# Optimization experiments

Measured on AMD Instinct MI355X. Metric: run time of the kernel, lower is better.

Reference implementation:

```python
import jax, jax.numpy as jnp
import numpy as np


def _knn_graph(x, k):
    """Faithful port of DynamicLstmGnn.knn_to_graph + get_u_v, returning the
    dense symmetrized edge-weight matrix [N, N] (the original re-sparsifies
    this same matrix via coalesce; nonzero extraction is data-dependent and
    not jit-able, so the dense matrix is the canonical output)."""
    N = x.shape[0]
    # negative squared euclidean distance: -||xi||^2 + 2 xi.xj - ||xj||^2
    xx = jnp.sum(x * x, axis=1, keepdims=True)          # [N, 1]
    inner = -2.0 * (x @ x.T)                              # [N, N]
    pairwise_distance = -xx - inner - xx.T                # [N, N], <= 0
    vals, idx = jax.lax.top_k(pairwise_distance, k)       # [N, k] largest (= closest)
    rows = jnp.repeat(jnp.arange(N), k)                   # idx_prime.flatten()
    # sparse COO -> to_dense (duplicate indices sum, matching torch.sparse)
    edges = jnp.zeros((N, N), dtype=x.dtype).at[rows, idx.ravel()].add(vals.ravel())
    edges_int = (edges > 0).astype(x.dtype)
    reflected_int = edges_int + edges_int.T
    reflected_edges = edges + edges.T
    denom = jnp.where(reflected_int == 0, jnp.ones((), x.dtype), reflected_int)
    edges = reflected_edges / denom
    diag = jnp.arange(N)
    edges = edges.at[diag, diag].set(0.0)                 # fill_diagonal_(0)
    return edges


def setup_inputs() -> dict:
    key = jax.random.key(0)
    x = jax.random.normal(key, (10000, 64), dtype=jnp.float32)
    return {"x": x, "k": 5}


def reference(x, k):
    return _knn_graph(x, k)
```

## Files before the change

### kernel.cpp

```cpp
#include <hip/hip_runtime.h>
#include <math.h>
#include <limits.h>

#define D 64
#define K 5
#define LK 8
#define GK 12
#define NSPLIT 16
#define NTILES 625
#define ROWBLK 157
#define NCOMP (ROWBLK * NSPLIT)
typedef unsigned int u32;
typedef unsigned long long u64;
typedef __bf16 bf16x8 __attribute__((ext_vector_type(8)));
typedef float  f32x4v __attribute__((ext_vector_type(4)));

__device__ __forceinline__ u32 med3u(u32 a, u32 b, u32 c) {
    u32 r;
    asm("v_med3_u32 %0, %1, %2, %3" : "=v"(r) : "v"(a), "v"(b), "v"(c));
    return r;
}

__device__ __forceinline__ u32 pack32(float v, int idx) {
    u32 u = __float_as_uint(v);
    u ^= ((u32)((int)u >> 31)) | 0x80000000u;
    return (u & 0xFFFFC000u) | ((~(u32)idx) & 0x3FFFu);
}
__device__ __forceinline__ int idx32(u32 key) { return (int)((~key) & 0x3FFFu); }

__device__ __forceinline__ u64 packKV(float v, int idx) {
    u32 u = __float_as_uint(v);
    u ^= ((u32)((int)u >> 31)) | 0x80000000u;
    return ((u64)u << 32) | (u32)(~idx);
}
__device__ __forceinline__ float unpackV(u64 key) {
    u32 hu = (u32)(key >> 32);
    return (hu & 0x80000000u) ? __uint_as_float(hu & 0x7fffffffu)
                              : __uint_as_float(~hu);
}

template<int LO, int LA, int LB, typename T>
__device__ __forceinline__ void mergeKeep(T a[LA], const T b[LB]) {
    T A[LA], B[LB], out[LO];
#pragma unroll
    for (int i = 0; i < LA; ++i) A[i] = a[i];
#pragma unroll
    for (int i = 0; i < LB; ++i) B[i] = b[i];
#pragma unroll
    for (int m = 0; m < LO; ++m) {
        bool ta = A[0] >= B[0];
        out[m] = ta ? A[0] : B[0];
#pragma unroll
        for (int i = 0; i < LA - 1; ++i) A[i] = ta ? A[i + 1] : A[i];
        A[LA - 1] = ta ? (T)0 : A[LA - 1];
#pragma unroll
        for (int i = 0; i < LB - 1; ++i) B[i] = ta ? B[i] : B[i + 1];
        B[LB - 1] = ta ? B[LB - 1] : (T)0;
    }
#pragma unroll
    for (int m = 0; m < LO; ++m) a[m] = out[m];
}

__global__ __launch_bounds__(256) void prep(
    const float* __restrict__ x, __bf16* __restrict__ xbA, float* __restrict__ xxf, int N)
{
    int g = blockIdx.x * 256 + threadIdx.x;
    const int REPACK = NTILES * 2 * 64;
    if (g < REPACK) {
        int tile = g >> 7;
        int rem  = g & 127;
        int kh   = rem >> 6;
        int lane = rem & 63;
        int q = lane >> 4, r = lane & 15;
        int row = tile * 16 + r;
        int k0  = kh * 32 + q * 8;
        const float4* p = (const float4*)(x + (size_t)row * D + k0);
        float4 v0 = p[0], v1 = p[1];
        bf16x8 o;
        o[0] = (__bf16)v0.x; o[1] = (__bf16)v0.y; o[2] = (__bf16)v0.z; o[3] = (__bf16)v0.w;
        o[4] = (__bf16)v1.x; o[5] = (__bf16)v1.y; o[6] = (__bf16)v1.z; o[7] = (__bf16)v1.w;
        ((bf16x8*)xbA)[g] = o;
        return;
    }
    int i = g - REPACK;
    if (i >= N) return;
    const float4* p = (const float4*)(x + (size_t)i * D);
    float s = 0.f;
#pragma unroll
    for (int t = 0; t < 16; ++t) {
        float4 v = p[t];
        s += v.x * v.x + v.y * v.y + v.z * v.z + v.w * v.w;
    }
    xxf[i] = s;
}

__global__ __launch_bounds__(256) void topk_zero_mfma(
    const __bf16* __restrict__ xbA, const float* __restrict__ xxf, int N,
    u32* __restrict__ wsK, float* __restrict__ outZ, long long totalF4,
    int nZero, int f4PerZ)
{
    const int bx  = blockIdx.x;
    const int tid = threadIdx.x;

    if (bx % 6 == 0) {
        int zid = bx / 6;
        if (zid >= nZero) return;
        long long s = (long long)zid * f4PerZ;
        long long e = s + f4PerZ; if (e > totalF4) e = totalF4;
        const f32x4v z = {0.f, 0.f, 0.f, 0.f};
        for (long long i = s + tid; i < e; i += 256)
            __builtin_nontemporal_store(z, (f32x4v*)(outZ + 4 * i));
        return;
    }

    const int cid = bx - (bx / 6 + 1);
    if (cid >= NCOMP) return;
    const int split = cid / ROWBLK;
    const int rb    = cid - split * ROWBLK;

    const int lane = tid & 63;
    const int wave = tid >> 6;
    const int l15  = lane & 15;
    const int q    = lane >> 4;
    const int r0 = rb * 64 + wave * 16;

    const bf16x8* fb = (const bf16x8*)xbA;

    int bt = r0 >> 4; if (bt > NTILES - 1) bt = NTILES - 1;
    const bf16x8 B0 = fb[bt * 128 + lane];
    const bf16x8 B1 = fb[bt * 128 + 64 + lane];

    const bf16x8* ap = fb + (size_t)split * 128 + lane;
    const float* xcp = xxf + split * 16 + q * 4;
    int cbase = split * 16 + q * 4;
    const int apBump = NSPLIT * 128;
    const int xcBump = NSPLIT * 16;

    u32 L[LK];
#pragma unroll
    for (int m = 0; m < LK; ++m) L[m] = 0u;

    for (int t = split; t < NTILES; t += NSPLIT) {
        const bf16x8 A0 = ap[0];
        const bf16x8 A1 = ap[64];
        const f32x4v xc = *(const f32x4v*)xcp;
        ap += apBump;
        xcp += xcBump;

        f32x4v acc = {0.f, 0.f, 0.f, 0.f};
        acc = __builtin_amdgcn_mfma_f32_16x16x32_bf16(A0, B0, acc, 0, 0, 0);
        acc = __builtin_amdgcn_mfma_f32_16x16x32_bf16(A1, B1, acc, 0, 0, 0);

#pragma unroll
        for (int v = 0; v < 4; ++v) {
            float dk = fmaf(-0.5f, xc[v], acc[v]);
            u32 key = pack32(dk, cbase + v);
            u32 n0 = max(L[0], key);
            u32 n1 = med3u(L[0], L[1], key);
            u32 n2 = med3u(L[1], L[2], key);
            u32 n3 = med3u(L[2], L[3], key);
            u32 n4 = med3u(L[3], L[4], key);
            u32 n5 = med3u(L[4], L[5], key);
            u32 n6 = med3u(L[5], L[6], key);
            u32 n7 = med3u(L[6], L[7], key);
            L[0]=n0; L[1]=n1; L[2]=n2; L[3]=n3; L[4]=n4; L[5]=n5; L[6]=n6; L[7]=n7;
        }
        cbase += xcBump;
    }

#pragma unroll
    for (int mask = 16; mask <= 32; mask <<= 1) {
        u32 P[LK];
#pragma unroll
        for (int m = 0; m < LK; ++m) P[m] = (u32)__shfl_xor((int)L[m], mask);
        mergeKeep<LK, LK, LK, u32>(L, P);
    }

    if (lane < 16) {
        int row = r0 + l15;
        if (row < N) {
            u32* dst = wsK + ((size_t)row * NSPLIT + split) * LK;
#pragma unroll
            for (int m = 0; m < LK; ++m) dst[m] = L[m];
        }
    }
}

__global__ __launch_bounds__(256) void rescore_scatter(
    const u32* __restrict__ wsK, const float* __restrict__ x, const float* __restrict__ xxf,
    float* __restrict__ out, int N)
{
    const int lane = threadIdx.x & 63;
    const int wave = threadIdx.x >> 6;
    const int sub  = lane & 3;
    const int row  = blockIdx.x * 64 + wave * 16 + (lane >> 2);
    const bool vrow = (row < N);
    const int rr = vrow ? row : 0;

    u32 cur[GK];
    {
        const u32* Lp = wsK + ((size_t)rr * NSPLIT + 4 * sub) * LK;
#pragma unroll
        for (int m = 0; m < LK; ++m) cur[m] = Lp[m];
#pragma unroll
        for (int m = LK; m < GK; ++m) cur[m] = 0u;
#pragma unroll
        for (int l = 1; l < 4; ++l) {
            u32 b[LK];
#pragma unroll
            for (int m = 0; m < LK; ++m) b[m] = Lp[l * LK + m];
            mergeKeep<GK, GK, LK, u32>(cur, b);
        }
    }
#pragma unroll
    for (int mask = 1; mask <= 2; mask <<= 1) {
        u32 P[GK];
#pragma unroll
        for (int m = 0; m < GK; ++m) P[m] = (u32)__shfl_xor((int)cur[m], mask);
        mergeKeep<GK, GK, GK, u32>(cur, P);
    }

    const float nxi = xxf[rr];
    int   cj[3]; bool cval[3];
    float d[3] = {0.f, 0.f, 0.f};
    const f32x4v* pj[3];
#pragma unroll
    for (int c = 0; c < 3; ++c) {
        int j = idx32(cur[sub * 3 + c]);
        cval[c] = (j < N) && (cur[sub * 3 + c] != 0u);
        cj[c] = cval[c] ? j : 0;
        pj[c] = (const f32x4v*)(x + (size_t)cj[c] * D);
    }
    const f32x4v* xip = (const f32x4v*)(x + (size_t)rr * D);
#pragma unroll
    for (int t = 0; t < 16; ++t) {
        const f32x4v xv = xip[t];
#pragma unroll
        for (int c = 0; c < 3; ++c) {
            const f32x4v pv = pj[c][t];
            d[c] = fmaf(xv[0], pv[0], d[c]);
            d[c] = fmaf(xv[1], pv[1], d[c]);
            d[c] = fmaf(xv[2], pv[2], d[c]);
            d[c] = fmaf(xv[3], pv[3], d[c]);
        }
    }
    u64 F[K];
#pragma unroll
    for (int c = 0; c < 3; ++c) {
        float val = 2.f * d[c] - nxi - xxf[cj[c]];
        F[c] = cval[c] ? packKV(val, cj[c]) : 0ull;
    }
    F[3] = 0ull; F[4] = 0ull;
    { u64 a0=F[0],a1=F[1],a2=F[2];
      if (a0 < a1) { u64 t0=a0; a0=a1; a1=t0; }
      if (a1 < a2) { u64 t0=a1; a1=a2; a2=t0; }
      if (a0 < a1) { u64 t0=a0; a0=a1; a1=t0; }
      F[0]=a0; F[1]=a1; F[2]=a2; }
#pragma unroll
    for (int mask = 1; mask <= 2; mask <<= 1) {
        u64 P[K];
#pragma unroll
        for (int m = 0; m < K; ++m) P[m] = __shfl_xor(F[m], mask);
        mergeKeep<K, K, K, u64>(F, P);
    }

    if (sub == 0 && vrow) {
#pragma unroll
        for (int m = 0; m < K; ++m) {
            int j = (int)(~(u32)F[m]);
            if ((unsigned)j < (unsigned)N && j != row) {
                float v = unpackV(F[m]);
                atomicAdd(out + (size_t)row * N + j, v);
                atomicAdd(out + (size_t)j * N + row, v);
            }
        }
    }
}

extern "C" void kernel_launch(void* const* d_in, const int* in_sizes, int n_in,
                              void* d_out, int out_size, void* d_ws, size_t ws_size,
                              hipStream_t stream) {
    const float* x = (const float*)d_in[0];
    const int N = in_sizes[0] / D;
    float* out = (float*)d_out;

    const size_t oXB = 0;
    const size_t oXX = ((size_t)NTILES * 2 * 64 * 8 * 2 + 255) & ~255ull;
    const size_t oWK = (oXX + (size_t)N * 4 + 255) & ~255ull;
    __bf16* xbA = (__bf16*)((char*)d_ws + oXB);
    float*  xxf = (float*)((char*)d_ws + oXX);
    u32*    wsK = (u32*)((char*)d_ws + oWK);

    const int prepThreads = NTILES * 2 * 64 + N;
    prep<<<(prepThreads + 255) / 256, 256, 0, stream>>>(x, xbA, xxf, N);

    long long totalF4 = (long long)out_size / 4;
    const int nBlocksTotal = 3024;
    const int nZero = (nBlocksTotal + 5) / 6;
    int f4PerZ = (int)((totalF4 + nZero - 1) / nZero);
    topk_zero_mfma<<<nBlocksTotal, 256, 0, stream>>>(
        xbA, xxf, N, wsK, out, totalF4, nZero, f4PerZ);

    rescore_scatter<<<ROWBLK, 256, 0, stream>>>(wsK, x, xxf, out, N);
}
```

Measured before the change: 451.2 us.

## Fuse top-k and rescore-scatter kernels with atomic-counter grid dependency

Merges the top-k/zeroing kernel and the rescore/scatter kernel into one launch. The trailing 157 blocks spin on two global completion counters, reset in prep, until all zeroing and top-k blocks have signalled. This removes one kernel launch boundary and the tail gap between them. In exchange it relies on forward progress of block scheduling: if the spinning blocks occupy slots ahead of producers they can delay them or deadlock. The threadfence plus atomic handshake also adds some overhead.

After: 951.7 us. 2.11x slower.

```diff
diff --git a/kernel.cpp b/kernel.cpp
--- a/kernel.cpp
+++ b/kernel.cpp
@@ -10,6 +10,8 @@
 #define NTILES 625
 #define ROWBLK 157
 #define NCOMP (ROWBLK * NSPLIT)
+#define NMIX  3024
+#define NZERO 504
 typedef unsigned int u32;
 typedef unsigned long long u64;
 typedef __bf16 bf16x8 __attribute__((ext_vector_type(8)));
@@ -62,9 +64,11 @@
 }
 
 __global__ __launch_bounds__(256) void prep(
-    const float* __restrict__ x, __bf16* __restrict__ xbA, float* __restrict__ xxf, int N)
+    const float* __restrict__ x, __bf16* __restrict__ xbA, float* __restrict__ xxf,
+    u32* __restrict__ ctrs, int N)
 {
     int g = blockIdx.x * 256 + threadIdx.x;
+    if (g < 2) ctrs[g] = 0u;
     const int REPACK = NTILES * 2 * 64;
     if (g < REPACK) {
         int tile = g >> 7;
@@ -94,108 +98,122 @@
     xxf[i] = s;
 }
 
-__global__ __launch_bounds__(256) void topk_zero_mfma(
-    const __bf16* __restrict__ xbA, const float* __restrict__ xxf, int N,
-    u32* __restrict__ wsK, float* __restrict__ outZ, long long totalF4,
-    int nZero, int f4PerZ)
+__global__ __launch_bounds__(256) void fused(
+    const __bf16* __restrict__ xbA, const float* __restrict__ xxf,
+    const float* __restrict__ x, int N,
+    u32* __restrict__ wsK, u32* __restrict__ ctrs,
+    float* __restrict__ outZ, long long totalF4, int f4PerZ)
 {
     const int bx  = blockIdx.x;
     const int tid = threadIdx.x;
 
-    if (bx % 6 == 0) {
+    if (bx < NMIX && bx % 6 == 0) {
         int zid = bx / 6;
-        if (zid >= nZero) return;
         long long s = (long long)zid * f4PerZ;
         long long e = s + f4PerZ; if (e > totalF4) e = totalF4;
         const f32x4v z = {0.f, 0.f, 0.f, 0.f};
         for (long long i = s + tid; i < e; i += 256)
             __builtin_nontemporal_store(z, (f32x4v*)(outZ + 4 * i));
+        __threadfence();
+        __syncthreads();
+        if (tid == 0) atomicAdd(&ctrs[0], 1u);
         return;
     }
 
-    const int cid = bx - (bx / 6 + 1);
-    if (cid >= NCOMP) return;
-    const int split = cid / ROWBLK;
-    const int rb    = cid - split * ROWBLK;
-
+    if (bx < NMIX) {
+        const int cid = bx - (bx / 6 + 1);
+        if (cid >= NCOMP) { __syncthreads(); if (tid == 0) atomicAdd(&ctrs[1], 1u); return; }
+        const int split = cid / ROWBLK;
+        const int rb    = cid - split * ROWBLK;
+
+        const int lane = tid & 63;
+        const int wave = tid >> 6;
+        const int l15  = lane & 15;
+        const int q    = lane >> 4;
+        const int r0 = rb * 64 + wave * 16;
+
+        const bf16x8* fb = (const bf16x8*)xbA;
+
+        int bt = r0 >> 4; if (bt > NTILES - 1) bt = NTILES - 1;
+        const bf16x8 B0 = fb[bt * 128 + lane];
+        const bf16x8 B1 = fb[bt * 128 + 64 + lane];
+
+        const bf16x8* ap = fb + (size_t)split * 128 + lane;
+        const float* xcp = xxf + split * 16 + q * 4;
+        int cbase = split * 16 + q * 4;
+        const int apBump = NSPLIT * 128;
+        const int xcBump = NSPLIT * 16;
+
+        u32 L[LK];
+#pragma unroll
+        for (int m = 0; m < LK; ++m) L[m] = 0u;
+
+        for (int t = split; t < NTILES; t += NSPLIT) {
+            const bf16x8 A0 = ap[0];
+            const bf16x8 A1 = ap[64];
+            const f32x4v xc = *(const f32x4v*)xcp;
+            ap += apBump;
+            xcp += xcBump;
+
+            f32x4v acc = {0.f, 0.f, 0.f, 0.f};
+            acc = __builtin_amdgcn_mfma_f32_16x16x32_bf16(A0, B0, acc, 0, 0, 0);
+            acc = __builtin_amdgcn_mfma_f32_16x16x32_bf16(A1, B1, acc, 0, 0, 0);
+
+#pragma unroll
+            for (int v = 0; v < 4; ++v) {
+                float dk = fmaf(-0.5f, xc[v], acc[v]);
+                u32 key = pack32(dk, cbase + v);
+                u32 n0 = max(L[0], key);
+                u32 n1 = med3u(L[0], L[1], key);
+                u32 n2 = med3u(L[1], L[2], key);
+                u32 n3 = med3u(L[2], L[3], key);
+                u32 n4 = med3u(L[3], L[4], key);
+                u32 n5 = med3u(L[4], L[5], key);
+                u32 n6 = med3u(L[5], L[6], key);
+                u32 n7 = med3u(L[6], L[7], key);
+                L[0]=n0; L[1]=n1; L[2]=n2; L[3]=n3; L[4]=n4; L[5]=n5; L[6]=n6; L[7]=n7;
+            }
+            cbase += xcBump;
+        }
+
+#pragma unroll
+        for (int mask = 16; mask <= 32; mask <<= 1) {
+            u32 P[LK];
+#pragma unroll
+            for (int m = 0; m < LK; ++m) P[m] = (u32)__shfl_xor((int)L[m], mask);
+            mergeKeep<LK, LK, LK, u32>(L, P);
+        }
+
+        if (lane < 16) {
+            int row = r0 + l15;
+            if (row < N) {
+                u32* dst = wsK + ((size_t)row * NSPLIT + split) * LK;
+#pragma unroll
+                for (int m = 0; m < LK; ++m) dst[m] = L[m];
+            }
+        }
+        __threadfence();
+        __syncthreads();
+        if (tid == 0) atomicAdd(&ctrs[1], 1u);
+        return;
+    }
+
+    if (tid == 0) {
+        while (__hip_atomic_load(&ctrs[0], __ATOMIC_ACQUIRE, __HIP_MEMORY_SCOPE_AGENT) < (u32)NZERO ||
+               __hip_atomic_load(&ctrs[1], __ATOMIC_ACQUIRE, __HIP_MEMORY_SCOPE_AGENT) < (u32)(NMIX - NZERO))
+            __builtin_amdgcn_s_sleep(8);
+    }
+    __syncthreads();
+    __threadfence();
+
+    const int rbx  = bx - NMIX;
     const int lane = tid & 63;
     const int wave = tid >> 6;
-    const int l15  = lane & 15;
-    const int q    = lane >> 4;
-    const int r0 = rb * 64 + wave * 16;
-
-    const bf16x8* fb = (const bf16x8*)xbA;
-
-    int bt = r0 >> 4; if (bt > NTILES - 1) bt = NTILES - 1;
-    const bf16x8 B0 = fb[bt * 128 + lane];
-    const bf16x8 B1 = fb[bt * 128 + 64 + lane];
-
-    const bf16x8* ap = fb + (size_t)split * 128 + lane;
-    const float* xcp = xxf + split * 16 + q * 4;
-    int cbase = split * 16 + q * 4;
-    const int apBump = NSPLIT * 128;
-    const int xcBump = NSPLIT * 16;
-
-    u32 L[LK];
-#pragma unroll
-    for (int m = 0; m < LK; ++m) L[m] = 0u;
-
-    for (int t = split; t < NTILES; t += NSPLIT) {
-        const bf16x8 A0 = ap[0];
-        const bf16x8 A1 = ap[64];
-        const f32x4v xc = *(const f32x4v*)xcp;
-        ap += apBump;
-        xcp += xcBump;
-
-        f32x4v acc = {0.f, 0.f, 0.f, 0.f};
-        acc = __builtin_amdgcn_mfma_f32_16x16x32_bf16(A0, B0, acc, 0, 0, 0);
-        acc = __builtin_amdgcn_mfma_f32_16x16x32_bf16(A1, B1, acc, 0, 0, 0);
-
-#pragma unroll
-        for (int v = 0; v < 4; ++v) {
-            float dk = fmaf(-0.5f, xc[v], acc[v]);
-            u32 key = pack32(dk, cbase + v);
-            u32 n0 = max(L[0], key);
-            u32 n1 = med3u(L[0], L[1], key);
-            u32 n2 = med3u(L[1], L[2], key);
-            u32 n3 = med3u(L[2], L[3], key);
-            u32 n4 = med3u(L[3], L[4], key);
-            u32 n5 = med3u(L[4], L[5], key);
-            u32 n6 = med3u(L[5], L[6], key);
-            u32 n7 = med3u(L[6], L[7], key);
-            L[0]=n0; L[1]=n1; L[2]=n2; L[3]=n3; L[4]=n4; L[5]=n5; L[6]=n6; L[7]=n7;
-        }
-        cbase += xcBump;
-    }
-
-#pragma unroll
-    for (int mask = 16; mask <= 32; mask <<= 1) {
-        u32 P[LK];
-#pragma unroll
-        for (int m = 0; m < LK; ++m) P[m] = (u32)__shfl_xor((int)L[m], mask);
-        mergeKeep<LK, LK, LK, u32>(L, P);
-    }
-
-    if (lane < 16) {
-        int row = r0 + l15;
-        if (row < N) {
-            u32* dst = wsK + ((size_t)row * NSPLIT + split) * LK;
-#pragma unroll
-            for (int m = 0; m < LK; ++m) dst[m] = L[m];
-        }
-    }
-}
-
-__global__ __launch_bounds__(256) void rescore_scatter(
-    const u32* __restrict__ wsK, const float* __restrict__ x, const float* __restrict__ xxf,
-    float* __restrict__ out, int N)
-{
-    const int lane = threadIdx.x & 63;
-    const int wave = threadIdx.x >> 6;
     const int sub  = lane & 3;
-    const int row  = blockIdx.x * 64 + wave * 16 + (lane >> 2);
+    const int row  = rbx * 64 + wave * 16 + (lane >> 2);
     const bool vrow = (row < N);
     const int rr = vrow ? row : 0;
+    float* out = outZ;
 
     u32 cur[GK];
     {
@@ -287,19 +305,17 @@
     const size_t oXB = 0;
     const size_t oXX = ((size_t)NTILES * 2 * 64 * 8 * 2 + 255) & ~255ull;
     const size_t oWK = (oXX + (size_t)N * 4 + 255) & ~255ull;
+    const size_t oCT = (oWK + (size_t)N * NSPLIT * LK * 4 + 255) & ~255ull;
     __bf16* xbA = (__bf16*)((char*)d_ws + oXB);
     float*  xxf = (float*)((char*)d_ws + oXX);
     u32*    wsK = (u32*)((char*)d_ws + oWK);
+    u32*    ctrs = (u32*)((char*)d_ws + oCT);
 
     const int prepThreads = NTILES * 2 * 64 + N;
-    prep<<<(prepThreads + 255) / 256, 256, 0, stream>>>(x, xbA, xxf, N);
+    prep<<<(prepThreads + 255) / 256, 256, 0, stream>>>(x, xbA, xxf, ctrs, N);
 
     long long totalF4 = (long long)out_size / 4;
-    const int nBlocksTotal = 3024;
-    const int nZero = (nBlocksTotal + 5) / 6;
-    int f4PerZ = (int)((totalF4 + nZero - 1) / nZero);
-    topk_zero_mfma<<<nBlocksTotal, 256, 0, stream>>>(
-        xbA, xxf, N, wsK, out, totalF4, nZero, f4PerZ);
-
-    rescore_scatter<<<ROWBLK, 256, 0, stream>>>(wsK, x, xxf, out, N);
-}
+    int f4PerZ = (int)((totalF4 + NZERO - 1) / NZERO);
+    fused<<<NMIX + ROWBLK, 256, 0, stream>>>(
+        xbA, xxf, x, N, wsK, ctrs, out, totalF4, f4PerZ);
+}
```
